# Optimization experiments

Hardware: AMD Instinct MI355X
Metric: run time of the kernel (lower is better)

Reference implementation:

```python
import jax, jax.numpy as jnp
import numpy as np

D_MODEL = 768
HEAD = 12
D_K = D_MODEL // HEAD


def setup_inputs() -> dict:
    key = jax.random.key(0)
    ks = jax.random.split(key, 9)
    s = 1.0 / np.sqrt(D_MODEL)
    return {
        "x": jax.random.normal(ks[0], (2, 4096, D_MODEL), dtype=jnp.float32),
        "Wq": jax.random.normal(ks[1], (D_MODEL, D_MODEL), dtype=jnp.float32) * s,
        "bq": jax.random.normal(ks[2], (D_MODEL,), dtype=jnp.float32) * 0.01,
        "Wk": jax.random.normal(ks[3], (D_MODEL, D_MODEL), dtype=jnp.float32) * s,
        "bk": jax.random.normal(ks[4], (D_MODEL,), dtype=jnp.float32) * 0.01,
        "Wv": jax.random.normal(ks[5], (D_MODEL, D_MODEL), dtype=jnp.float32) * s,
        "bv": jax.random.normal(ks[6], (D_MODEL,), dtype=jnp.float32) * 0.01,
        "Wo": jax.random.normal(ks[7], (D_MODEL, D_MODEL), dtype=jnp.float32) * s,
        "bo": jax.random.normal(ks[8], (D_MODEL,), dtype=jnp.float32) * 0.01,
    }


def reference(x, Wq, bq, Wk, bk, Wv, bv, Wo, bo):
    B, S, _ = x.shape
    # Linear projections, split into heads: [B, H, S, d_k]
    def proj(W, b):
        return (x @ W + b).reshape(B, S, HEAD, D_K).transpose(0, 2, 1, 3)
    Q, K, V = proj(Wq, bq), proj(Wk, bk), proj(Wv, bv)
    scale = 1.0 / jnp.sqrt(jnp.asarray(D_K, x.dtype))
    # [B, H, S, S] attention scores (materialized, as in the original module)
    scores = jnp.einsum('bhqd,bhkd->bhqk', Q, K) * scale
    probs = jax.nn.softmax(scores, axis=-1)  # dropout is identity in eval mode
    ctx = jnp.einsum('bhqk,bhkd->bhqd', probs, V)
    ctx = ctx.transpose(0, 2, 1, 3).reshape(B, S, D_MODEL)
    return ctx @ Wo + bo
```

## Files before the change

kernel.cpp:

```cpp
#include <hip/hip_runtime.h>

#define D_MODEL 768
#define S_LEN   4096
#define NHEAD   12
#define DK      64
#define TKA     64

typedef _Float16 f16;
typedef _Float16 f16x8 __attribute__((ext_vector_type(8)));
typedef _Float16 f16x4 __attribute__((ext_vector_type(4)));
typedef __fp16   fp16x2 __attribute__((ext_vector_type(2)));
typedef float    f32x4 __attribute__((ext_vector_type(4)));

#define MFMA16(a, b, c) __builtin_amdgcn_mfma_f32_16x16x32_f16(a, b, c, 0, 0, 0)

#define Q_PRESCALE 0.18033688f
#define SOFTMAX_C  11.54156036f

__device__ inline f16x8 ldf(const f16* p) {
    return *reinterpret_cast<const f16x8*>(p);
}

__device__ inline void gl2lds16(const f16* g, f16* l) {
    __builtin_amdgcn_global_load_lds(
        (const __attribute__((address_space(1))) void*)g,
        (__attribute__((address_space(3))) void*)l, 16, 0, 0);
}

__global__ __launch_bounds__(256) void cvt_x_kernel(const float* __restrict__ x,
                                                    f16* __restrict__ xb) {
    size_t i = ((size_t)blockIdx.x * 256 + threadIdx.x) * 4;
    float4 v = *reinterpret_cast<const float4*>(x + i);
    f16x4 o = { (f16)v.x, (f16)v.y, (f16)v.z, (f16)v.w };
    *reinterpret_cast<f16x4*>(xb + i) = o;
}

__global__ __launch_bounds__(256) void wtrans_kernel(const float* __restrict__ Wq,
                                                     const float* __restrict__ Wk,
                                                     const float* __restrict__ Wv,
                                                     const float* __restrict__ Wo,
                                                     f16* __restrict__ WT) {
    const int z = blockIdx.z;
    const float* in = (z == 0) ? Wq : (z == 1) ? Wk : (z == 2) ? Wv : Wo;
    f16* out = WT + (size_t)z * D_MODEL * D_MODEL;
    __shared__ float tile[32][33];
    const int tx = threadIdx.x, ty = threadIdx.y;
    const int n0 = blockIdx.x * 32, k0 = blockIdx.y * 32;
#pragma unroll
    for (int j = 0; j < 32; j += 8)
        tile[ty + j][tx] = in[(size_t)(k0 + ty + j) * D_MODEL + n0 + tx];
    __syncthreads();
#pragma unroll
    for (int j = 0; j < 32; j += 8)
        out[(size_t)(n0 + ty + j) * D_MODEL + k0 + tx] = (f16)tile[tx][ty + j];
}

__global__ __launch_bounds__(256, 3) void gemm_qkv_kernel(
        const f16* __restrict__ A, const f16* __restrict__ WT,
        const float* __restrict__ bq, const float* __restrict__ bk,
        const float* __restrict__ bv,
        f16* __restrict__ Qb, f16* __restrict__ Kb, f16* __restrict__ Vt) {
    __shared__ __align__(16) f16 asmem[3][128 * 32];
    __shared__ __align__(16) f16 bsmem[3][128 * 32];
    const int z = blockIdx.z;
    const f16* Bt = WT + (size_t)z * D_MODEL * D_MODEL;
    const float* bias = (z == 0) ? bq : (z == 1) ? bk : bv;
    const int w = threadIdx.x >> 6;
    const int lane = threadIdx.x & 63;
    const int ln = lane & 15, quad = lane >> 4;
    const int mb = blockIdx.x * 128;
    const int nb = blockIdx.y * 128;
    const int mloc = (w & 1) * 64, nloc = (w >> 1) * 64;
    const int l0 = w * 64 + lane;

    auto stage = [&](int buf, int kb) {
#pragma unroll
        for (int p = 0; p < 2; p++) {
            const int l = p * 256 + l0;
            gl2lds16(A + (size_t)(mb + (l >> 2)) * D_MODEL + kb + (l & 3) * 8,
                     &asmem[buf][(p * 256 + w * 64) * 8]);
        }
#pragma unroll
        for (int p = 0; p < 2; p++) {
            const int l = p * 256 + l0;
            gl2lds16(Bt + (size_t)(nb + (l >> 2)) * D_MODEL + kb + (l & 3) * 8,
                     &bsmem[buf][(p * 256 + w * 64) * 8]);
        }
    };

    f32x4 acc[4][4] = {};
    stage(0, 0);
    stage(1, 32);
    __syncthreads();

    const int NIT = D_MODEL / 32;
    int cb = 0, sb = 2;
    for (int it = 0; it < NIT; ++it) {
        f16x8 af[4], bf[4];
#pragma unroll
        for (int i = 0; i < 4; i++)
            af[i] = ldf(&asmem[cb][(mloc + i * 16 + ln) * 32 + quad * 8]);
#pragma unroll
        for (int t = 0; t < 4; t++)
            bf[t] = ldf(&bsmem[cb][(nloc + t * 16 + ln) * 32 + quad * 8]);
#pragma unroll
        for (int i = 0; i < 4; i++)
#pragma unroll
            for (int t = 0; t < 4; t++)
                acc[i][t] = MFMA16(af[i], bf[t], acc[i][t]);
        __syncthreads();
        if (it + 2 < NIT) stage(sb, (it + 2) * 32);
        cb = (cb == 2) ? 0 : cb + 1;
        sb = (sb == 2) ? 0 : sb + 1;
    }

#pragma unroll
    for (int t = 0; t < 4; t++) {
        const int n = nb + nloc + t * 16 + ln;
        const float bval = bias[n];
        const int h = n >> 6, d = n & 63;
#pragma unroll
        for (int i = 0; i < 4; i++) {
            const int m = mb + mloc + i * 16 + quad * 4;
            const int b = m >> 12, s = m & 4095;
            const int bh = b * NHEAD + h;
            if (z == 0) {
#pragma unroll
                for (int r = 0; r < 4; r++)
                    Qb[((size_t)bh * S_LEN + s + r) * DK + d] =
                        (f16)((acc[i][t][r] + bval) * Q_PRESCALE);
            } else if (z == 1) {
#pragma unroll
                for (int r = 0; r < 4; r++)
                    Kb[((size_t)bh * S_LEN + s + r) * DK + d] =
                        (f16)(acc[i][t][r] + bval);
            } else {
                f16x4 pk;
#pragma unroll
                for (int r = 0; r < 4; r++) pk[r] = (f16)(acc[i][t][r] + bval);
                *reinterpret_cast<f16x4*>(&Vt[((size_t)bh * DK + d) * S_LEN + s]) = pk;
            }
        }
    }
}

__global__ __launch_bounds__(256, 2) void attn_kernel(const f16* __restrict__ Qb,
                                                      const f16* __restrict__ Kb,
                                                      const f16* __restrict__ Vt,
                                                      f16* __restrict__ Ctx) {
    __shared__ __align__(16) f16 kbuf[3][TKA * DK];
    __shared__ __align__(16) f16 vbuf[3][DK * TKA];
    __shared__ __align__(16) f16 plds[4][32][72];

    const int w = threadIdx.x >> 6;
    const int lane = threadIdx.x & 63;
    const int ln = lane & 15, quad = lane >> 4;

    const int blk = blockIdx.x;
    const int xcd = blk & 7, sidx = blk >> 3;
    const int bh = xcd * 3 + (sidx >> 5);
    const int qb = (sidx & 31) * 128;
    const int b = bh / NHEAD, h = bh % NHEAD;

    const f16* Kbh = Kb + (size_t)bh * S_LEN * DK;
    const f16* Vbh = Vt + (size_t)bh * DK * S_LEN;

    f16x8 aq[2][2];
#pragma unroll
    for (int i2 = 0; i2 < 2; i2++) {
        const f16* qp = Qb + ((size_t)bh * S_LEN + qb + w * 32 + i2 * 16 + ln) * DK;
        aq[i2][0] = ldf(qp + quad * 8);
        aq[i2][1] = ldf(qp + 32 + quad * 8);
    }

    int rS[2], cS[2];
#pragma unroll
    for (int p = 0; p < 2; p++) {
        const int l = p * 256 + w * 64 + lane;
        const int r = l >> 3;
        rS[p] = r;
        cS[p] = ((l & 7) - r - (r >> 3)) & 7;
    }

    auto stage = [&](int buf, int kk) {
#pragma unroll
        for (int p = 0; p < 2; p++)
            gl2lds16(Kbh + (size_t)(kk + rS[p]) * DK + cS[p] * 8,
                     &kbuf[buf][(p * 256 + w * 64) * 8]);
#pragma unroll
        for (int p = 0; p < 2; p++)
            gl2lds16(Vbh + (size_t)rS[p] * S_LEN + kk + cS[p] * 8,
                     &vbuf[buf][(p * 256 + w * 64) * 8]);
    };

    f32x4 acc[2][4] = {};
    f32x4 lsum[2] = {};

    stage(0, 0);
    stage(1, TKA);
    __syncthreads();

    const int NIT = S_LEN / TKA;
    int cb = 0, sb = 2;
    for (int it = 0; it < NIT; ++it) {
        const f16* kb = kbuf[cb];
        const f16* vb = vbuf[cb];

        f16x8 kf[4][2];
#pragma unroll
        for (int t = 0; t < 4; t++) {
            const int rr = 4 * ln + t;
            const int sw = rr + (rr >> 3);
#pragma unroll
            for (int hh = 0; hh < 2; hh++)
                kf[t][hh] = ldf(kb + rr * DK + (((hh * 4 + quad + sw) & 7) * 8));
        }

        f32x4 s[2][4];
#pragma unroll
        for (int i2 = 0; i2 < 2; i2++)
#pragma unroll
            for (int t = 0; t < 4; t++) {
                f32x4 si = { -SOFTMAX_C, -SOFTMAX_C, -SOFTMAX_C, -SOFTMAX_C };
                si = MFMA16(aq[i2][0], kf[t][0], si);
                si = MFMA16(aq[i2][1], kf[t][1], si);
                s[i2][t] = si;
            }

#pragma unroll
        for (int i2 = 0; i2 < 2; i2++)
#pragma unroll
            for (int r = 0; r < 4; r++) {
                const float e0 = __builtin_amdgcn_exp2f(s[i2][0][r]);
                const float e1 = __builtin_amdgcn_exp2f(s[i2][1][r]);
                const float e2 = __builtin_amdgcn_exp2f(s[i2][2][r]);
                const float e3 = __builtin_amdgcn_exp2f(s[i2][3][r]);
                lsum[i2][r] += (e0 + e1) + (e2 + e3);
                union { fp16x2 h2[2]; unsigned long long u; } pk;
                pk.h2[0] = __builtin_amdgcn_cvt_pkrtz(e0, e1);
                pk.h2[1] = __builtin_amdgcn_cvt_pkrtz(e2, e3);
                *reinterpret_cast<unsigned long long*>(
                    &plds[w][i2 * 16 + quad * 4 + r][4 * ln]) = pk.u;
            }
        __builtin_amdgcn_wave_barrier();

        f16x8 ap[2][2];
#pragma unroll
        for (int i2 = 0; i2 < 2; i2++)
#pragma unroll
            for (int hh = 0; hh < 2; hh++)
                ap[i2][hh] = ldf(&plds[w][i2 * 16 + ln][hh * 32 + quad * 8]);

#pragma unroll
        for (int t = 0; t < 4; t++) {
            const int rr = t * 16 + ln;
            const int sw = rr + (rr >> 3);
            const f16x8 vf0 = ldf(vb + rr * DK + (((quad + sw) & 7) * 8));
            const f16x8 vf1 = ldf(vb + rr * DK + (((4 + quad + sw) & 7) * 8));
#pragma unroll
            for (int i2 = 0; i2 < 2; i2++) {
                acc[i2][t] = MFMA16(ap[i2][0], vf0, acc[i2][t]);
                acc[i2][t] = MFMA16(ap[i2][1], vf1, acc[i2][t]);
            }
        }

        __syncthreads();
        if (it + 2 < NIT) stage(sb, (it + 2) * TKA);
        cb = (cb == 2) ? 0 : cb + 1;
        sb = (sb == 2) ? 0 : sb + 1;
    }

#pragma unroll
    for (int i2 = 0; i2 < 2; i2++)
#pragma unroll
        for (int r = 0; r < 4; r++) {
            float l = lsum[i2][r];
            l += __shfl_xor(l, 1, 16);
            l += __shfl_xor(l, 2, 16);
            l += __shfl_xor(l, 4, 16);
            l += __shfl_xor(l, 8, 16);
            const float rl = 1.0f / l;
            const int q = qb + w * 32 + i2 * 16 + quad * 4 + r;
#pragma unroll
            for (int t = 0; t < 4; t++)
                Ctx[((size_t)b * S_LEN + q) * D_MODEL + h * DK + t * 16 + ln] =
                    (f16)(acc[i2][t][r] * rl);
        }
}

__global__ __launch_bounds__(256, 3) void gemm_o_kernel(const f16* __restrict__ A,
                                                        const f16* __restrict__ Bt,
                                                        const float* __restrict__ bo,
                                                        float* __restrict__ out) {
    __shared__ __align__(16) f16 asmem[3][128 * 32];
    __shared__ __align__(16) f16 bsmem[3][128 * 32];
    const int w = threadIdx.x >> 6;
    const int lane = threadIdx.x & 63;
    const int ln = lane & 15, quad = lane >> 4;
    const int mb = blockIdx.x * 128;
    const int nb = blockIdx.y * 128;
    const int mloc = (w & 1) * 64, nloc = (w >> 1) * 64;
    const int l0 = w * 64 + lane;

    auto stage = [&](int buf, int kb) {
#pragma unroll
        for (int p = 0; p < 2; p++) {
            const int l = p * 256 + l0;
            gl2lds16(A + (size_t)(mb + (l >> 2)) * D_MODEL + kb + (l & 3) * 8,
                     &asmem[buf][(p * 256 + w * 64) * 8]);
        }
#pragma unroll
        for (int p = 0; p < 2; p++) {
            const int l = p * 256 + l0;
            gl2lds16(Bt + (size_t)(nb + (l >> 2)) * D_MODEL + kb + (l & 3) * 8,
                     &bsmem[buf][(p * 256 + w * 64) * 8]);
        }
    };

    f32x4 acc[4][4] = {};
    stage(0, 0);
    stage(1, 32);
    __syncthreads();

    const int NIT = D_MODEL / 32;
    int cb = 0, sb = 2;
    for (int it = 0; it < NIT; ++it) {
        f16x8 af[4], bf[4];
#pragma unroll
        for (int i = 0; i < 4; i++)
            af[i] = ldf(&asmem[cb][(mloc + i * 16 + ln) * 32 + quad * 8]);
#pragma unroll
        for (int t = 0; t < 4; t++)
            bf[t] = ldf(&bsmem[cb][(nloc + t * 16 + ln) * 32 + quad * 8]);
#pragma unroll
        for (int i = 0; i < 4; i++)
#pragma unroll
            for (int t = 0; t < 4; t++)
                acc[i][t] = MFMA16(af[i], bf[t], acc[i][t]);
        __syncthreads();
        if (it + 2 < NIT) stage(sb, (it + 2) * 32);
        cb = (cb == 2) ? 0 : cb + 1;
        sb = (sb == 2) ? 0 : sb + 1;
    }

#pragma unroll
    for (int t = 0; t < 4; t++) {
        const int n = nb + nloc + t * 16 + ln;
        const float bval = bo[n];
#pragma unroll
        for (int i = 0; i < 4; i++) {
            const int m = mb + mloc + i * 16 + quad * 4;
#pragma unroll
            for (int r = 0; r < 4; r++)
                out[(size_t)(m + r) * D_MODEL + n] = acc[i][t][r] + bval;
        }
    }
}

extern "C" void kernel_launch(void* const* d_in, const int* in_sizes, int n_in,
                              void* d_out, int out_size, void* d_ws, size_t ws_size,
                              hipStream_t stream) {
    const float* x  = (const float*)d_in[0];
    const float* Wq = (const float*)d_in[1];
    const float* bq = (const float*)d_in[2];
    const float* Wk = (const float*)d_in[3];
    const float* bk = (const float*)d_in[4];
    const float* Wv = (const float*)d_in[5];
    const float* bv = (const float*)d_in[6];
    const float* Wo = (const float*)d_in[7];
    const float* bo = (const float*)d_in[8];
    float* out = (float*)d_out;

    f16* ws = (f16*)d_ws;
    f16* Xb  = ws;
    f16* Ctx = ws;
    f16* WT  = ws + 6291456;
    f16* Qb  = ws + 8650752;
    f16* Kb  = ws + 14942208;
    f16* Vt  = ws + 21233664;

    cvt_x_kernel<<<6144, 256, 0, stream>>>(x, Xb);
    wtrans_kernel<<<dim3(24, 24, 4), dim3(32, 8), 0, stream>>>(Wq, Wk, Wv, Wo, WT);
    gemm_qkv_kernel<<<dim3(64, 6, 3), 256, 0, stream>>>(Xb, WT, bq, bk, bv, Qb, Kb, Vt);
    attn_kernel<<<768, 256, 0, stream>>>(Qb, Kb, Vt, Ctx);
    gemm_o_kernel<<<dim3(64, 6), 256, 0, stream>>>(Ctx, WT + (size_t)3 * D_MODEL * D_MODEL, bo, out);
}
```

Baseline: 309.2 us.

## Compute transposed scores to keep softmax probabilities in registers, dropping LDS round-trip

```diff
diff --git a/kernel.cpp b/kernel.cpp
--- a/kernel.cpp
+++ b/kernel.cpp
@@ -144,13 +144,12 @@
     }
 }
 
-__global__ __launch_bounds__(256, 2) void attn_kernel(const f16* __restrict__ Qb,
+__global__ __launch_bounds__(256, 3) void attn_kernel(const f16* __restrict__ Qb,
                                                       const f16* __restrict__ Kb,
                                                       const f16* __restrict__ Vt,
                                                       f16* __restrict__ Ctx) {
     __shared__ __align__(16) f16 kbuf[3][TKA * DK];
     __shared__ __align__(16) f16 vbuf[3][DK * TKA];
-    __shared__ __align__(16) f16 plds[4][32][72];
 
     const int w = threadIdx.x >> 6;
     const int lane = threadIdx.x & 63;
@@ -173,28 +172,29 @@
         aq[i2][1] = ldf(qp + 32 + quad * 8);
     }
 
-    int rS[2], cS[2];
+    int rS[2], ckS[2], cvS[2];
 #pragma unroll
     for (int p = 0; p < 2; p++) {
         const int l = p * 256 + w * 64 + lane;
         const int r = l >> 3;
-        rS[p] = r;
-        cS[p] = ((l & 7) - r - (r >> 3)) & 7;
+        rS[p]  = r;
+        ckS[p] = ((l & 7) - r - (r >> 2)) & 7;
+        cvS[p] = ((l & 7) - r - (r >> 3)) & 7;
     }
 
     auto stage = [&](int buf, int kk) {
 #pragma unroll
         for (int p = 0; p < 2; p++)
-            gl2lds16(Kbh + (size_t)(kk + rS[p]) * DK + cS[p] * 8,
+            gl2lds16(Kbh + (size_t)(kk + rS[p]) * DK + ckS[p] * 8,
                      &kbuf[buf][(p * 256 + w * 64) * 8]);
 #pragma unroll
         for (int p = 0; p < 2; p++)
-            gl2lds16(Vbh + (size_t)rS[p] * S_LEN + kk + cS[p] * 8,
+            gl2lds16(Vbh + (size_t)rS[p] * S_LEN + kk + cvS[p] * 8,
                      &vbuf[buf][(p * 256 + w * 64) * 8]);
     };
 
-    f32x4 acc[2][4] = {};
-    f32x4 lsum[2] = {};
+    f32x4 acc[4][2] = {};
+    float lsum[2] = {0.f, 0.f};
 
     stage(0, 0);
     stage(1, TKA);
@@ -206,61 +206,42 @@
         const f16* kb = kbuf[cb];
         const f16* vb = vbuf[cb];
 
-        f16x8 kf[4][2];
-#pragma unroll
-        for (int t = 0; t < 4; t++) {
-            const int rr = 4 * ln + t;
-            const int sw = rr + (rr >> 3);
-#pragma unroll
-            for (int hh = 0; hh < 2; hh++)
-                kf[t][hh] = ldf(kb + rr * DK + (((hh * 4 + quad + sw) & 7) * 8));
-        }
-
-        f32x4 s[2][4];
-#pragma unroll
-        for (int i2 = 0; i2 < 2; i2++)
-#pragma unroll
-            for (int t = 0; t < 4; t++) {
-                f32x4 si = { -SOFTMAX_C, -SOFTMAX_C, -SOFTMAX_C, -SOFTMAX_C };
-                si = MFMA16(aq[i2][0], kf[t][0], si);
-                si = MFMA16(aq[i2][1], kf[t][1], si);
-                s[i2][t] = si;
+        union { f16x8 v; fp16x2 h2[4]; } pb[2][2];
+
+#pragma unroll
+        for (int kt = 0; kt < 2; kt++) {
+#pragma unroll
+            for (int a = 0; a < 2; a++) {
+                const int rr = kt * 32 + 8 * (ln >> 2) + 4 * a + (ln & 3);
+                const int sw = rr + (rr >> 2);
+                const f16x8 kf0 = ldf(kb + rr * DK + (((quad + sw) & 7) * 8));
+                const f16x8 kf1 = ldf(kb + rr * DK + (((quad + 4 + sw) & 7) * 8));
+#pragma unroll
+                for (int i2 = 0; i2 < 2; i2++) {
+                    f32x4 si = { -SOFTMAX_C, -SOFTMAX_C, -SOFTMAX_C, -SOFTMAX_C };
+                    si = MFMA16(kf0, aq[i2][0], si);
+                    si = MFMA16(kf1, aq[i2][1], si);
+                    const float e0 = __builtin_amdgcn_exp2f(si[0]);
+                    const float e1 = __builtin_amdgcn_exp2f(si[1]);
+                    const float e2 = __builtin_amdgcn_exp2f(si[2]);
+                    const float e3 = __builtin_amdgcn_exp2f(si[3]);
+                    lsum[i2] += (e0 + e1) + (e2 + e3);
+                    pb[kt][i2].h2[2 * a]     = __builtin_amdgcn_cvt_pkrtz(e0, e1);
+                    pb[kt][i2].h2[2 * a + 1] = __builtin_amdgcn_cvt_pkrtz(e2, e3);
+                }
             }
-
-#pragma unroll
-        for (int i2 = 0; i2 < 2; i2++)
-#pragma unroll
-            for (int r = 0; r < 4; r++) {
-                const float e0 = __builtin_amdgcn_exp2f(s[i2][0][r]);
-                const float e1 = __builtin_amdgcn_exp2f(s[i2][1][r]);
-                const float e2 = __builtin_amdgcn_exp2f(s[i2][2][r]);
-                const float e3 = __builtin_amdgcn_exp2f(s[i2][3][r]);
-                lsum[i2][r] += (e0 + e1) + (e2 + e3);
-                union { fp16x2 h2[2]; unsigned long long u; } pk;
-                pk.h2[0] = __builtin_amdgcn_cvt_pkrtz(e0, e1);
-                pk.h2[1] = __builtin_amdgcn_cvt_pkrtz(e2, e3);
-                *reinterpret_cast<unsigned long long*>(
-                    &plds[w][i2 * 16 + quad * 4 + r][4 * ln]) = pk.u;
-            }
-        __builtin_amdgcn_wave_barrier();
-
-        f16x8 ap[2][2];
-#pragma unroll
-        for (int i2 = 0; i2 < 2; i2++)
-#pragma unroll
-            for (int hh = 0; hh < 2; hh++)
-                ap[i2][hh] = ldf(&plds[w][i2 * 16 + ln][hh * 32 + quad * 8]);
+        }
 
 #pragma unroll
         for (int t = 0; t < 4; t++) {
             const int rr = t * 16 + ln;
             const int sw = rr + (rr >> 3);
-            const f16x8 vf0 = ldf(vb + rr * DK + (((quad + sw) & 7) * 8));
-            const f16x8 vf1 = ldf(vb + rr * DK + (((4 + quad + sw) & 7) * 8));
-#pragma unroll
-            for (int i2 = 0; i2 < 2; i2++) {
-                acc[i2][t] = MFMA16(ap[i2][0], vf0, acc[i2][t]);
-                acc[i2][t] = MFMA16(ap[i2][1], vf1, acc[i2][t]);
+#pragma unroll
+            for (int kt = 0; kt < 2; kt++) {
+                const f16x8 vf = ldf(vb + rr * TKA + (((quad + 4 * kt + sw) & 7) * 8));
+#pragma unroll
+                for (int i2 = 0; i2 < 2; i2++)
+                    acc[t][i2] = MFMA16(vf, pb[kt][i2].v, acc[t][i2]);
             }
         }
 
@@ -271,21 +252,21 @@
     }
 
 #pragma unroll
-    for (int i2 = 0; i2 < 2; i2++)
-#pragma unroll
-        for (int r = 0; r < 4; r++) {
-            float l = lsum[i2][r];
-            l += __shfl_xor(l, 1, 16);
-            l += __shfl_xor(l, 2, 16);
-            l += __shfl_xor(l, 4, 16);
-            l += __shfl_xor(l, 8, 16);
-            const float rl = 1.0f / l;
-            const int q = qb + w * 32 + i2 * 16 + quad * 4 + r;
-#pragma unroll
-            for (int t = 0; t < 4; t++)
-                Ctx[((size_t)b * S_LEN + q) * D_MODEL + h * DK + t * 16 + ln] =
-                    (f16)(acc[i2][t][r] * rl);
-        }
+    for (int i2 = 0; i2 < 2; i2++) {
+        float l = lsum[i2];
+        l += __shfl_xor(l, 16, 64);
+        l += __shfl_xor(l, 32, 64);
+        const float rl = 1.0f / l;
+        const int q = qb + w * 32 + i2 * 16 + ln;
+        f16* cp = Ctx + ((size_t)b * S_LEN + q) * D_MODEL + h * DK + 4 * quad;
+#pragma unroll
+        for (int t = 0; t < 4; t++) {
+            f16x4 pk;
+#pragma unroll
+            for (int r = 0; r < 4; r++) pk[r] = (f16)(acc[t][i2][r] * rl);
+            *reinterpret_cast<f16x4*>(cp + t * 16) = pk;
+        }
+    }
 }
 
 __global__ __launch_bounds__(256, 3) void gemm_o_kernel(const f16* __restrict__ A,
```

Result: faster. 278.2 us (-10.0%).
